# Optimization experiments

Measured on AMD Instinct MI355X. Metric: run time of the kernel, lower is better.

The kernel has to match this reference:

```python
import jax, jax.numpy as jnp
import numpy as np

NUM_GRAPHS = 64
GRAPH_SIZE = 1024   # nodes per graph (equal-sized graphs -> batched form of the per-graph loop)
PROJ_DIM = 64       # ProjectionHead output_dim default
TEMPERATURE = 0.5   # GRACE default


def setup_inputs() -> dict:
    key = jax.random.key(0)
    k1, k2 = jax.random.split(key)
    N = NUM_GRAPHS * GRAPH_SIZE
    z1 = jax.random.normal(k1, (N, PROJ_DIM), dtype=jnp.float32)
    z2 = jax.random.normal(k2, (N, PROJ_DIM), dtype=jnp.float32)
    # batch assignment: graph ids, sorted, equal-sized graphs
    batch = jnp.repeat(jnp.arange(NUM_GRAPHS, dtype=jnp.int64), GRAPH_SIZE)
    return {"z1": z1, "z2": z2, "batch": batch, "num_graphs": NUM_GRAPHS}


def _node_nt_xent(z1, z2, num_graphs, temperature):
    # z1, z2: [N, d] projected node embeddings; equal-sized graphs of G nodes.
    N, d = z1.shape
    G = N // num_graphs
    # F.normalize(dim=1)
    z1 = z1 / jnp.linalg.norm(z1, axis=1, keepdims=True)
    z2 = z2 / jnp.linalg.norm(z2, axis=1, keepdims=True)
    z1g = z1.reshape(num_graphs, G, d)  # [B, G, d]
    z2g = z2.reshape(num_graphs, G, d)
    inv_t = 1.0 / temperature
    # within-graph similarity matrices [B, G, G]
    sim12 = jnp.einsum('bid,bjd->bij', z1g, z2g) * inv_t
    sim11 = jnp.einsum('bid,bjd->bij', z1g, z1g) * inv_t
    # positive = diag(sim12)
    pos = jnp.einsum('bid,bid->bi', z1g, z2g) * inv_t  # [B, G]
    eye = jnp.eye(G, dtype=bool)
    neg12 = jnp.where(eye, -jnp.inf, sim12)
    neg11 = jnp.where(eye, -jnp.inf, sim11)
    # cross-entropy with label 0 on logits = [pos | neg12 | neg11]
    # = logsumexp(all logits) - pos  (done without materializing the concat)
    lse12 = jax.nn.logsumexp(neg12, axis=-1)  # [B, G]
    lse11 = jax.nn.logsumexp(neg11, axis=-1)
    lse = jax.nn.logsumexp(jnp.stack([pos, lse12, lse11], axis=-1), axis=-1)
    # sum_g mean_g * n_g / N  ==  global mean over nodes
    return jnp.mean(lse - pos)


def reference(z1, z2, batch, num_graphs):
    # batch is consistent with equal-sized, sorted graph ids (see setup_inputs);
    # the ragged per-graph python loop collapses to one batched computation.
    return _node_nt_xent(z1, z2, int(num_graphs), TEMPERATURE)
```

## Files before the change

### kernel.cpp

```cpp
#include <hip/hip_runtime.h>
#include <hip/hip_bf16.h>

#define N_NODES 65536
#define NUM_G   64
#define GSIZE   1024
#define DIM     64

using frag_ab = __attribute__((ext_vector_type(8))) short;
using f32x4   = __attribute__((ext_vector_type(4))) float;

__device__ __forceinline__ unsigned short f2bf(float x) {
    union { float f; unsigned int u; } v; v.f = x;
    unsigned int r = v.u + 0x7FFFu + ((v.u >> 16) & 1u);
    return (unsigned short)(r >> 16);
}

__global__ __launch_bounds__(256) void normalize_k(
    const float* __restrict__ z1, const float* __restrict__ z2,
    unsigned short* __restrict__ z1n, unsigned short* __restrict__ z2n,
    float* __restrict__ pos)
{
    int tid = threadIdx.x;
    int row = blockIdx.x * 16 + (tid >> 4);
    int l4  = tid & 15;
    float4 v1 = *((const float4*)(z1 + (size_t)row * DIM) + l4);
    float4 v2 = *((const float4*)(z2 + (size_t)row * DIM) + l4);
    float ss1 = v1.x*v1.x + v1.y*v1.y + v1.z*v1.z + v1.w*v1.w;
    float ss2 = v2.x*v2.x + v2.y*v2.y + v2.z*v2.z + v2.w*v2.w;
    float dt  = v1.x*v2.x + v1.y*v2.y + v1.z*v2.z + v1.w*v2.w;
    #pragma unroll
    for (int m = 1; m < 16; m <<= 1) {
        ss1 += __shfl_xor(ss1, m);
        ss2 += __shfl_xor(ss2, m);
        dt  += __shfl_xor(dt,  m);
    }
    float in1 = 1.0f / sqrtf(ss1);
    float in2 = 1.0f / sqrtf(ss2);
    ushort4 o1, o2;
    o1.x = f2bf(v1.x*in1); o1.y = f2bf(v1.y*in1); o1.z = f2bf(v1.z*in1); o1.w = f2bf(v1.w*in1);
    o2.x = f2bf(v2.x*in2); o2.y = f2bf(v2.y*in2); o2.z = f2bf(v2.z*in2); o2.w = f2bf(v2.w*in2);
    *((ushort4*)(z1n + (size_t)row * DIM) + l4) = o1;
    *((ushort4*)(z2n + (size_t)row * DIM) + l4) = o2;
    if (l4 == 0) pos[row] = dt * in1 * in2 * 2.0f;
}

__global__ __launch_bounds__(512, 4) void grace_main_k(
    const unsigned short* __restrict__ z1n,
    const unsigned short* __restrict__ z2n,
    const float* __restrict__ pos,
    float* __restrict__ partials)
{
    __shared__ unsigned short smem[2][128 * 64];
    __shared__ float red[8];

    int tid = threadIdx.x;
    int n = blockIdx.x;
    int g = (n & 7) + 8 * (n >> 6);
    int stripe = (n >> 3) & 7;
    int w = tid >> 6, l = tid & 63;
    const unsigned short* z1g = z1n + (size_t)g * GSIZE * DIM;
    const unsigned short* z2g = z2n + (size_t)g * GSIZE * DIM;
    int rowBase = stripe * 128 + w * 16;

    int ar = l & 15, ak = (l >> 4) * 8;
    frag_ab a0 = *(const frag_ab*)(z1g + (rowBase + ar) * DIM +  0 + ak);
    frag_ab a1 = *(const frag_ab*)(z1g + (rowBase + ar) * DIM + 32 + ak);

    float expacc[4] = {};

    int col0 = tid >> 3, slot = tid & 7;
    int col1 = col0 + 64;
    int off0 = ((col0 << 7) + (slot << 4)) ^ ((col0 & 7) << 4);
    int off1 = ((col1 << 7) + (slot << 4)) ^ ((col1 & 7) << 4);

    auto src_ptr = [&](int p, int c) -> const int4* {
        int j = p * 128 + c;
        const unsigned short* s = (j < 1024) ? (z2g + j * DIM) : (z1g + (j - 1024) * DIM);
        return (const int4*)(s + slot * 8);
    };

    int bcol = l & 15, bgrp = l >> 4, bx = (l & 7) << 4;

    const float K1 = 2.8853900817779268f;
    const float K0 = -2.8853900817779268f;

    int4 pre0 = *src_ptr(0, col0);
    int4 pre1 = *src_ptr(0, col1);
    *(int4*)((char*)smem[0] + off0) = pre0;
    *(int4*)((char*)smem[0] + off1) = pre1;
    __syncthreads();

    #pragma unroll 1
    for (int i = 0; i < 16; ++i) {
        if (i < 15) {
            pre0 = *src_ptr(i + 1, col0);
            pre1 = *src_ptr(i + 1, col1);
        }
        const char* base = (const char*)smem[i & 1];
        #pragma unroll
        for (int ct = 0; ct < 8; ++ct) {
            int col = ct * 16 + bcol;
            frag_ab b0 = *(const frag_ab*)(base + (((col << 7) + (bgrp << 4)) ^ bx));
            frag_ab b1 = *(const frag_ab*)(base + (((col << 7) + ((4 + bgrp) << 4)) ^ bx));
            f32x4 z = {0.f, 0.f, 0.f, 0.f};
            f32x4 c = __builtin_amdgcn_mfma_f32_16x16x32_bf16(a0, b0, z, 0, 0, 0);
            c = __builtin_amdgcn_mfma_f32_16x16x32_bf16(a1, b1, c, 0, 0, 0);
            #pragma unroll
            for (int r = 0; r < 4; ++r)
                expacc[r] += __builtin_amdgcn_exp2f(fmaf(c[r], K1, K0));
        }
        if (i < 15) {
            char* wb = (char*)smem[(i + 1) & 1];
            *(int4*)(wb + off0) = pre0;
            *(int4*)(wb + off1) = pre1;
            __syncthreads();
        }
    }

    float part = 0.f;
    #pragma unroll
    for (int r = 0; r < 4; ++r) {
        float s = expacc[r];
        s += __shfl_xor(s, 1); s += __shfl_xor(s, 2);
        s += __shfl_xor(s, 4); s += __shfl_xor(s, 8);
        if ((l & 15) == 0) {
            int row = rowBase + (l >> 4) * 4 + r;
            part += 2.0f + __logf(s - 1.0f) - pos[g * GSIZE + row];
        }
    }
    #pragma unroll
    for (int m = 1; m < 64; m <<= 1) part += __shfl_xor(part, m);
    if (l == 0) red[w] = part;
    __syncthreads();
    if (tid == 0) {
        float s = 0.f;
        #pragma unroll
        for (int k = 0; k < 8; ++k) s += red[k];
        partials[blockIdx.x] = s;
    }
}

__global__ __launch_bounds__(256) void final_reduce_k(
    const float* __restrict__ partials, float* __restrict__ out)
{
    int tid = threadIdx.x;
    float s = partials[tid] + partials[tid + 256];
    #pragma unroll
    for (int m = 1; m < 64; m <<= 1) s += __shfl_xor(s, m);
    __shared__ float red[4];
    if ((tid & 63) == 0) red[tid >> 6] = s;
    __syncthreads();
    if (tid == 0) out[0] = (red[0] + red[1] + red[2] + red[3]) * (1.0f / N_NODES);
}

extern "C" void kernel_launch(void* const* d_in, const int* in_sizes, int n_in,
                              void* d_out, int out_size, void* d_ws, size_t ws_size,
                              hipStream_t stream)
{
    const float* z1 = (const float*)d_in[0];
    const float* z2 = (const float*)d_in[1];
    char* ws = (char*)d_ws;
    unsigned short* z1n = (unsigned short*)ws;
    unsigned short* z2n = (unsigned short*)(ws + 8388608);
    float* pos          = (float*)(ws + 16777216);
    float* partials     = (float*)(ws + 17039360);

    normalize_k<<<dim3(N_NODES / 16), dim3(256), 0, stream>>>(z1, z2, z1n, z2n, pos);
    grace_main_k<<<dim3(NUM_G * 8), dim3(512), 0, stream>>>(z1n, z2n, pos, partials);
    final_reduce_k<<<dim3(1), dim3(256), 0, stream>>>(partials, (float*)d_out);
}
```

Measured before the change: 45.48 us.

## Hold all A row tiles in registers and stream B from global without LDS

The main kernel now uses 256-thread blocks. Each wave keeps all eight 16-row A tiles of the block's 128-row stripe in registers and walks a disjoint quarter of the 2048 candidate columns, loading B fragments straight from global memory with one-step register prefetch. This removes the LDS double buffer and its per-tile barriers, and reuses each B fragment across eight MFMA row tiles. Per-wave partial exp sums are combined through shared memory at the end. The cost is much higher register pressure (A fragments plus 32 accumulators), fewer resident waves, and less latency hiding for global loads that now go through cache instead of LDS.

```diff
diff --git a/kernel.cpp b/kernel.cpp
--- a/kernel.cpp
+++ b/kernel.cpp
@@ -44,14 +44,14 @@
     if (l4 == 0) pos[row] = dt * in1 * in2 * 2.0f;
 }
 
-__global__ __launch_bounds__(512, 4) void grace_main_k(
+__global__ __launch_bounds__(256, 3) void grace_main_k(
     const unsigned short* __restrict__ z1n,
     const unsigned short* __restrict__ z2n,
     const float* __restrict__ pos,
     float* __restrict__ partials)
 {
-    __shared__ unsigned short smem[2][128 * 64];
-    __shared__ float red[8];
+    __shared__ float sums[4][128];
+    __shared__ float red[4];
 
     int tid = threadIdx.x;
     int n = blockIdx.x;
@@ -60,84 +60,71 @@
     int w = tid >> 6, l = tid & 63;
     const unsigned short* z1g = z1n + (size_t)g * GSIZE * DIM;
     const unsigned short* z2g = z2n + (size_t)g * GSIZE * DIM;
-    int rowBase = stripe * 128 + w * 16;
+    int rowBase = stripe * 128;
 
     int ar = l & 15, ak = (l >> 4) * 8;
-    frag_ab a0 = *(const frag_ab*)(z1g + (rowBase + ar) * DIM +  0 + ak);
-    frag_ab a1 = *(const frag_ab*)(z1g + (rowBase + ar) * DIM + 32 + ak);
+    frag_ab A[8][2];
+    #pragma unroll
+    for (int rt = 0; rt < 8; ++rt) {
+        const unsigned short* p = z1g + (rowBase + rt * 16 + ar) * DIM + ak;
+        A[rt][0] = *(const frag_ab*)(p);
+        A[rt][1] = *(const frag_ab*)(p + 32);
+    }
 
-    float expacc[4] = {};
+    float expacc[8][4] = {};
 
-    int col0 = tid >> 3, slot = tid & 7;
-    int col1 = col0 + 64;
-    int off0 = ((col0 << 7) + (slot << 4)) ^ ((col0 & 7) << 4);
-    int off1 = ((col1 << 7) + (slot << 4)) ^ ((col1 & 7) << 4);
-
-    auto src_ptr = [&](int p, int c) -> const int4* {
-        int j = p * 128 + c;
-        const unsigned short* s = (j < 1024) ? (z2g + j * DIM) : (z1g + (j - 1024) * DIM);
-        return (const int4*)(s + slot * 8);
-    };
-
-    int bcol = l & 15, bgrp = l >> 4, bx = (l & 7) << 4;
+    const unsigned short* sb =
+        ((w < 2) ? z2g : z1g) + ((w & 1) * 512 + ar) * DIM + ak;
 
     const float K1 = 2.8853900817779268f;
     const float K0 = -2.8853900817779268f;
 
-    int4 pre0 = *src_ptr(0, col0);
-    int4 pre1 = *src_ptr(0, col1);
-    *(int4*)((char*)smem[0] + off0) = pre0;
-    *(int4*)((char*)smem[0] + off1) = pre1;
+    frag_ab b0 = *(const frag_ab*)(sb);
+    frag_ab b1 = *(const frag_ab*)(sb + 32);
+    sb += 16 * DIM;
+
+    #pragma unroll 1
+    for (int t = 0; t < 32; ++t) {
+        frag_ab nb0, nb1;
+        if (t < 31) {
+            nb0 = *(const frag_ab*)(sb);
+            nb1 = *(const frag_ab*)(sb + 32);
+            sb += 16 * DIM;
+        }
+        #pragma unroll
+        for (int rt = 0; rt < 8; ++rt) {
+            f32x4 z = {0.f, 0.f, 0.f, 0.f};
+            f32x4 c = __builtin_amdgcn_mfma_f32_16x16x32_bf16(A[rt][0], b0, z, 0, 0, 0);
+            c = __builtin_amdgcn_mfma_f32_16x16x32_bf16(A[rt][1], b1, c, 0, 0, 0);
+            #pragma unroll
+            for (int r = 0; r < 4; ++r)
+                expacc[rt][r] += __builtin_amdgcn_exp2f(fmaf(c[r], K1, K0));
+        }
+        if (t < 31) { b0 = nb0; b1 = nb1; }
+    }
+
+    #pragma unroll
+    for (int rt = 0; rt < 8; ++rt) {
+        #pragma unroll
+        for (int r = 0; r < 4; ++r) {
+            float s = expacc[rt][r];
+            s += __shfl_xor(s, 1); s += __shfl_xor(s, 2);
+            s += __shfl_xor(s, 4); s += __shfl_xor(s, 8);
+            if ((l & 15) == 0) sums[w][rt * 16 + (l >> 4) * 4 + r] = s;
+        }
+    }
     __syncthreads();
 
-    #pragma unroll 1
-    for (int i = 0; i < 16; ++i) {
-        if (i < 15) {
-            pre0 = *src_ptr(i + 1, col0);
-            pre1 = *src_ptr(i + 1, col1);
-        }
-        const char* base = (const char*)smem[i & 1];
-        #pragma unroll
-        for (int ct = 0; ct < 8; ++ct) {
-            int col = ct * 16 + bcol;
-            frag_ab b0 = *(const frag_ab*)(base + (((col << 7) + (bgrp << 4)) ^ bx));
-            frag_ab b1 = *(const frag_ab*)(base + (((col << 7) + ((4 + bgrp) << 4)) ^ bx));
-            f32x4 z = {0.f, 0.f, 0.f, 0.f};
-            f32x4 c = __builtin_amdgcn_mfma_f32_16x16x32_bf16(a0, b0, z, 0, 0, 0);
-            c = __builtin_amdgcn_mfma_f32_16x16x32_bf16(a1, b1, c, 0, 0, 0);
-            #pragma unroll
-            for (int r = 0; r < 4; ++r)
-                expacc[r] += __builtin_amdgcn_exp2f(fmaf(c[r], K1, K0));
-        }
-        if (i < 15) {
-            char* wb = (char*)smem[(i + 1) & 1];
-            *(int4*)(wb + off0) = pre0;
-            *(int4*)(wb + off1) = pre1;
-            __syncthreads();
-        }
-    }
-
-    float part = 0.f;
-    #pragma unroll
-    for (int r = 0; r < 4; ++r) {
-        float s = expacc[r];
-        s += __shfl_xor(s, 1); s += __shfl_xor(s, 2);
-        s += __shfl_xor(s, 4); s += __shfl_xor(s, 8);
-        if ((l & 15) == 0) {
-            int row = rowBase + (l >> 4) * 4 + r;
-            part += 2.0f + __logf(s - 1.0f) - pos[g * GSIZE + row];
-        }
+    float term = 0.f;
+    if (tid < 128) {
+        float S = sums[0][tid] + sums[1][tid] + sums[2][tid] + sums[3][tid];
+        term = 2.0f + __logf(S - 1.0f) - pos[g * GSIZE + rowBase + tid];
     }
     #pragma unroll
-    for (int m = 1; m < 64; m <<= 1) part += __shfl_xor(part, m);
-    if (l == 0) red[w] = part;
+    for (int m = 1; m < 64; m <<= 1) term += __shfl_xor(term, m);
+    if (l == 0) red[w] = term;
     __syncthreads();
-    if (tid == 0) {
-        float s = 0.f;
-        #pragma unroll
-        for (int k = 0; k < 8; ++k) s += red[k];
-        partials[blockIdx.x] = s;
-    }
+    if (tid == 0) partials[n] = red[0] + red[1] + red[2] + red[3];
 }
 
 __global__ __launch_bounds__(256) void final_reduce_k(
@@ -166,6 +153,6 @@
     float* partials     = (float*)(ws + 17039360);
 
     normalize_k<<<dim3(N_NODES / 16), dim3(256), 0, stream>>>(z1, z2, z1n, z2n, pos);
-    grace_main_k<<<dim3(NUM_G * 8), dim3(512), 0, stream>>>(z1n, z2n, pos, partials);
+    grace_main_k<<<dim3(NUM_G * 8), dim3(256), 0, stream>>>(z1n, z2n, pos, partials);
     final_reduce_k<<<dim3(1), dim3(256), 0, stream>>>(partials, (float*)d_out);
 }
```

Result: slower. 46.63 us (+2.5%).
